# Kernel optimization log

Measured on AMD Instinct MI355X. Metric: run time of the kernel, lower is better.

## Reference

```python
import jax, jax.numpy as jnp
import numpy as np

B, N, C = 2, 2048, 1024
H = 16
D = C // H  # head_dim = 64
SCALE = D ** -0.5


def setup_inputs() -> dict:
    key = jax.random.key(0)
    ks = jax.random.split(key, 9)
    s = C ** -0.5  # ~ torch Linear default init scale
    return {
        "x": jax.random.normal(ks[0], (B, N, C), dtype=jnp.float32),
        "Wq": jax.random.uniform(ks[1], (C, C), jnp.float32, -s, s),
        "bq": jax.random.uniform(ks[2], (C,), jnp.float32, -s, s),
        "Wk": jax.random.uniform(ks[3], (C, C), jnp.float32, -s, s),
        "bk": jax.random.uniform(ks[4], (C,), jnp.float32, -s, s),
        "Wv": jax.random.uniform(ks[5], (C, C), jnp.float32, -s, s),
        "bv": jax.random.uniform(ks[6], (C,), jnp.float32, -s, s),
        "Wo": jax.random.uniform(ks[7], (C, C), jnp.float32, -s, s),
        "bo": jax.random.uniform(ks[8], (C,), jnp.float32, -s, s),
    }


def reference(x, Wq, bq, Wk, bk, Wv, bv, Wo, bo):
    # Projections: [B,N,C] -> [B,H,N,D]
    def split_heads(t):
        return t.reshape(B, N, H, D).transpose(0, 2, 1, 3)

    q = split_heads(x @ Wq.T + bq)
    k = split_heads(x @ Wk.T + bk)
    v = split_heads(x @ Wv.T + bv)

    scores = jnp.einsum("bhnd,bhmd->bhnm", q, k) * SCALE  # [B,H,N,N]
    attn = jax.nn.softmax(scores, axis=-1)
    out = jnp.einsum("bhnm,bhmd->bhnd", attn, v)  # [B,H,N,D]
    out = out.transpose(0, 2, 1, 3).reshape(B, N, C)
    return out @ Wo.T + bo
```

## Files before the change

kernel.cpp:

```cpp
#include <hip/hip_runtime.h>
#include <stdint.h>


typedef _Float16 h8 __attribute__((ext_vector_type(8)));
typedef _Float16 h4 __attribute__((ext_vector_type(4)));
typedef float f4 __attribute__((ext_vector_type(4)));
typedef float f16f __attribute__((ext_vector_type(16)));
typedef uint32_t u32;
typedef u32 u32x4 __attribute__((ext_vector_type(4)));

#define AS1(p) ((const __attribute__((address_space(1))) void*)(p))
#define AS3(p) ((__attribute__((address_space(3))) void*)(p))

template <int ITERS>
__device__ __forceinline__ void stage128B(const _Float16* g, int ldk, _Float16* s, int tid) {
#pragma unroll
  for (int j = 0; j < ITERS; ++j) {
    int off = j * 4096 + tid * 16;
    int row = off >> 7;
    int ch = (off >> 4) & 7;
    int gch = ch ^ (row & 7);
    __builtin_amdgcn_global_load_lds(AS1(g + row * ldk + gch * 8), AS3(s + (off >> 1)), 16, 0, 0);
  }
}

__device__ __forceinline__ void stage_v(const _Float16* g, _Float16* s, int tid) {
#pragma unroll
  for (int j = 0; j < 2; ++j) {
    int off = j * 4096 + tid * 16;
    int row = off >> 7;
    int ch = (off >> 4) & 7;
    int gch = ch ^ (row & 7);
    __builtin_amdgcn_global_load_lds(AS1(g + row * 2048 + gch * 8), AS3(s + (off >> 1)), 16, 0, 0);
  }
}
__device__ __forceinline__ void stage_k(const _Float16* g, _Float16* s, int tid) {
#pragma unroll
  for (int j = 0; j < 2; ++j) {
    int off = j * 4096 + tid * 16;
    int row = off >> 7;
    int ch = (off >> 4) & 7;
    int gch = ch ^ ((row & 3) | ((row >> 1) & 4));
    __builtin_amdgcn_global_load_lds(AS1(g + row * 64 + gch * 8), AS3(s + (off >> 1)), 16, 0, 0);
  }
}

__device__ __forceinline__ h8 frag64(const _Float16* s, int row, int g) {
  return *(const h8*)(s + row * 64 + ((g ^ (row & 7)) << 3));
}

__global__ void cvt_all(const float* __restrict__ x, const float* __restrict__ Wq,
                        const float* __restrict__ Wk, const float* __restrict__ Wv,
                        const float* __restrict__ Wo, _Float16* __restrict__ xh,
                        _Float16* __restrict__ q, _Float16* __restrict__ k,
                        _Float16* __restrict__ v, _Float16* __restrict__ o) {
  int blk = blockIdx.x;
  const float* src; _Float16* dst; int off;
  if (blk < 4096)      { src = x;  dst = xh; off = blk; }
  else if (blk < 5120) { src = Wq; dst = q;  off = blk - 4096; }
  else if (blk < 6144) { src = Wk; dst = k;  off = blk - 5120; }
  else if (blk < 7168) { src = Wv; dst = v;  off = blk - 6144; }
  else                 { src = Wo; dst = o;  off = blk - 7168; }
  int i = off * 1024 + threadIdx.x * 4;
  f4 vv = *(const f4*)(src + i);
  h4 ov;
  ov[0] = (_Float16)vv[0]; ov[1] = (_Float16)vv[1]; ov[2] = (_Float16)vv[2]; ov[3] = (_Float16)vv[3];
  *(h4*)(dst + i) = ov;
}

__global__ __launch_bounds__(256, 3) void gemm_qkv(
    const _Float16* __restrict__ X,
    const _Float16* __restrict__ W0, const _Float16* __restrict__ W1, const _Float16* __restrict__ W2,
    const float* __restrict__ b0, const float* __restrict__ b1, const float* __restrict__ b2,
    _Float16* __restrict__ O0, _Float16* __restrict__ O1, _Float16* __restrict__ O2) {
  __shared__ _Float16 As[128 * 64];
  __shared__ _Float16 Bs[128 * 64];
  int z = blockIdx.z;
  const _Float16* W = (z == 0) ? W0 : (z == 1) ? W1 : W2;
  const float* bias = (z == 0) ? b0 : (z == 1) ? b1 : b2;

  int tid = threadIdx.x;
  int lane = tid & 63, wave = tid >> 6;
  int quad = lane >> 4, l15 = lane & 15;
  int wm = (wave >> 1) << 6, wn = (wave & 1) << 6;
  int m0 = blockIdx.y << 7, n0 = blockIdx.x << 7;

  f4 acc[4][4] = {};
  for (int k0 = 0; k0 < 1024; k0 += 64) {
    stage128B<4>(X + m0 * 1024 + k0, 1024, As, tid);
    stage128B<4>(W + n0 * 1024 + k0, 1024, Bs, tid);
    __syncthreads();
#pragma unroll
    for (int ks = 0; ks < 2; ++ks) {
      h8 af[4], bf[4];
#pragma unroll
      for (int i = 0; i < 4; ++i) af[i] = frag64(As, wm + i * 16 + l15, ks * 4 + quad);
#pragma unroll
      for (int i = 0; i < 4; ++i) bf[i] = frag64(Bs, wn + i * 16 + l15, ks * 4 + quad);
#pragma unroll
      for (int mi = 0; mi < 4; ++mi)
#pragma unroll
        for (int ni = 0; ni < 4; ++ni)
          acc[mi][ni] = __builtin_amdgcn_mfma_f32_16x16x32_f16(af[mi], bf[ni], acc[mi][ni], 0, 0, 0);
    }
    __syncthreads();
  }

  if (z == 2) {
#pragma unroll
    for (int mi = 0; mi < 4; ++mi) {
#pragma unroll
      for (int ni = 0; ni < 4; ++ni) {
        int o = n0 + wn + ni * 16 + l15;
        float bv = bias[o];
        int h = o >> 6, dd = o & 63;
        int m = m0 + wm + mi * 16 + quad * 4;
        int b = m >> 11, n = m & 2047;
        h4 v;
#pragma unroll
        for (int r = 0; r < 4; ++r) v[r] = (_Float16)(acc[mi][ni][r] + bv);
        *(h4*)(O2 + (((b * 16 + h) * 64 + dd) * 2048 + n)) = v;
      }
    }
  } else {
    float scale = (z == 0) ? 0.125f * 1.44269504089f : 1.0f;
    _Float16* Out = (z == 0) ? O0 : O1;
#pragma unroll
    for (int mi = 0; mi < 4; ++mi) {
#pragma unroll
      for (int ni = 0; ni < 4; ++ni) {
        int o = n0 + wn + ni * 16 + l15;
        float bv = bias[o];
        int h = o >> 6, d = o & 63;
#pragma unroll
        for (int r = 0; r < 4; ++r) {
          int m = m0 + wm + mi * 16 + quad * 4 + r;
          int b = m >> 11, n = m & 2047;
          float v = (acc[mi][ni][r] + bv) * scale;
          Out[(((b * 16 + h) * 2048 + n) << 6) + d] = (_Float16)v;
        }
      }
    }
  }
}

__global__ __launch_bounds__(256, 3) void gemm_out(
    const _Float16* __restrict__ A, const _Float16* __restrict__ W,
    const float* __restrict__ bias, float* __restrict__ Out) {
  __shared__ _Float16 As[128 * 64];
  __shared__ _Float16 Bs[64 * 64];
  int tid = threadIdx.x;
  int lane = tid & 63, wave = tid >> 6;
  int quad = lane >> 4, l15 = lane & 15;
  int wm = (wave >> 1) << 6, wn = (wave & 1) << 5;
  int m0 = blockIdx.y << 7, n0 = blockIdx.x << 6;

  f4 acc[4][2] = {};
  for (int k0 = 0; k0 < 1024; k0 += 64) {
    stage128B<4>(A + m0 * 1024 + k0, 1024, As, tid);
    stage128B<2>(W + n0 * 1024 + k0, 1024, Bs, tid);
    __syncthreads();
#pragma unroll
    for (int ks = 0; ks < 2; ++ks) {
      h8 af[4], bf[2];
#pragma unroll
      for (int i = 0; i < 4; ++i) af[i] = frag64(As, wm + i * 16 + l15, ks * 4 + quad);
#pragma unroll
      for (int i = 0; i < 2; ++i) bf[i] = frag64(Bs, wn + i * 16 + l15, ks * 4 + quad);
#pragma unroll
      for (int mi = 0; mi < 4; ++mi)
#pragma unroll
        for (int ni = 0; ni < 2; ++ni)
          acc[mi][ni] = __builtin_amdgcn_mfma_f32_16x16x32_f16(af[mi], bf[ni], acc[mi][ni], 0, 0, 0);
    }
    __syncthreads();
  }
#pragma unroll
  for (int mi = 0; mi < 4; ++mi) {
#pragma unroll
    for (int ni = 0; ni < 2; ++ni) {
      int o = n0 + wn + ni * 16 + l15;
      float bv = bias[o];
#pragma unroll
      for (int r = 0; r < 4; ++r) {
        int m = m0 + wm + mi * 16 + quad * 4 + r;
        Out[m * 1024 + o] = acc[mi][ni][r] + bv;
      }
    }
  }
}

__global__ __launch_bounds__(256, 2) void attn(
    const _Float16* __restrict__ Q, const _Float16* __restrict__ Kv,
    const _Float16* __restrict__ Vt, _Float16* __restrict__ AO) {
  __shared__ _Float16 smem[8 * 4096];
  _Float16* Ksb = smem;
  _Float16* Vsb = smem + 4 * 4096;

  int tid = threadIdx.x, lane = tid & 63, wave = tid >> 6;
  int h = lane >> 5, l31 = lane & 31;
  int p = wave & 1, qg = wave >> 1;

  int flat = blockIdx.y * 16 + blockIdx.x;
  int nid = (flat & 7) * 64 + (flat >> 3);
  int bh = nid >> 4, q0 = (nid & 15) << 7;

  const _Float16* Qb = Q + (bh * 2048 + q0 + qg * 64 + l31) * 64;
  h8 qf[2][4];
#pragma unroll
  for (int qs = 0; qs < 2; ++qs)
#pragma unroll
    for (int ks4 = 0; ks4 < 4; ++ks4)
      qf[qs][ks4] = *(const h8*)(Qb + qs * 32 * 64 + ks4 * 16 + h * 8);

  int krow = (l31 & 19) | ((l31 & 4) << 1) | ((l31 & 8) >> 1);
  int kbase = (p * 32 + krow) * 64;
  int kx = (krow & 3) | ((krow >> 1) & 4);
  int vx = l31 & 7;

  const _Float16* Kb = Kv + bh * 131072;
  const _Float16* Vb = Vt + bh * 131072;

  f16f zero = {};
  f16f oacc[2][2] = {};
  float lsum0 = 0.f, lsum1 = 0.f;

  auto SMPV = [&](const f16f& sa, const f16f& sb, const _Float16* Vst) {
    u32 pkw0[8], pkw1[8];
#pragma unroll
    for (int i = 0; i < 8; ++i) {
      float pa = __builtin_amdgcn_exp2f(sa[2 * i]);
      float pb = __builtin_amdgcn_exp2f(sa[2 * i + 1]);
      lsum0 += pa + pb;
      pkw0[i] = __builtin_bit_cast(u32, __builtin_amdgcn_cvt_pkrtz(pa, pb));
      float pc = __builtin_amdgcn_exp2f(sb[2 * i]);
      float pd = __builtin_amdgcn_exp2f(sb[2 * i + 1]);
      lsum1 += pc + pd;
      pkw1[i] = __builtin_bit_cast(u32, __builtin_amdgcn_cvt_pkrtz(pc, pd));
    }
#pragma unroll
    for (int s = 0; s < 2; ++s) {
      u32x4 pw0 = {pkw0[4 * s], pkw0[4 * s + 1], pkw0[4 * s + 2], pkw0[4 * s + 3]};
      u32x4 pw1 = {pkw1[4 * s], pkw1[4 * s + 1], pkw1[4 * s + 2], pkw1[4 * s + 3]};
      h8 pb0 = __builtin_bit_cast(h8, pw0);
      h8 pb1 = __builtin_bit_cast(h8, pw1);
      int ch = (((p << 2) | (s << 1) | h) ^ vx) << 3;
      __builtin_amdgcn_s_setprio(1);
#pragma unroll
      for (int dt = 0; dt < 2; ++dt) {
        h8 vf = *(const h8*)(Vst + (dt * 32 + l31) * 64 + ch);
        oacc[0][dt] = __builtin_amdgcn_mfma_f32_32x32x16_f16(vf, pb0, oacc[0][dt], 0, 0, 0);
        oacc[1][dt] = __builtin_amdgcn_mfma_f32_32x32x16_f16(vf, pb1, oacc[1][dt], 0, 0, 0);
      }
      __builtin_amdgcn_s_setprio(0);
    }
  };

  auto QK = [&](const _Float16* Kst, f16f& s0, f16f& s1) {
    s0 = zero; s1 = zero;
    __builtin_amdgcn_s_setprio(1);
#pragma unroll
    for (int ks4 = 0; ks4 < 4; ++ks4) {
      h8 kf = *(const h8*)(Kst + kbase + (((ks4 * 2 + h) ^ kx) << 3));
      s0 = __builtin_amdgcn_mfma_f32_32x32x16_f16(kf, qf[0][ks4], s0, 0, 0, 0);
      s1 = __builtin_amdgcn_mfma_f32_32x32x16_f16(kf, qf[1][ks4], s1, 0, 0, 0);
    }
    __builtin_amdgcn_s_setprio(0);
  };

  stage_k(Kb, Ksb, tid);
  stage_v(Vb, Vsb, tid);
  stage_k(Kb + 4096, Ksb + 4096, tid);
  stage_v(Vb + 64, Vsb + 4096, tid);

  f16f sA0 = zero, sA1 = zero, sB0 = zero, sB1 = zero;

  for (int it = 0; it < 16; ++it) {
    int base = (it & 1) << 1;
    int ob = base ^ 2;
    int ph0 = it << 1;

    asm volatile("s_waitcnt vmcnt(4)\n\ts_barrier" ::: "memory");
    if (it < 15) {
      stage_k(Kb + (ph0 + 2) * 4096, Ksb + ob * 4096, tid);
      stage_v(Vb + (ph0 + 2) * 64, Vsb + ob * 4096, tid);
    }
    QK(Ksb + base * 4096, sA0, sA1);
    if (it > 0) SMPV(sB0, sB1, Vsb + (ob | 1) * 4096);

    if (it < 15) {
      asm volatile("s_waitcnt vmcnt(4)\n\ts_barrier" ::: "memory");
      stage_k(Kb + (ph0 + 3) * 4096, Ksb + (ob | 1) * 4096, tid);
      stage_v(Vb + (ph0 + 3) * 64, Vsb + (ob | 1) * 4096, tid);
    } else {
      asm volatile("s_waitcnt vmcnt(0)\n\ts_barrier" ::: "memory");
    }
    QK(Ksb + (base | 1) * 4096, sB0, sB1);
    SMPV(sA0, sA1, Vsb + base * 4096);
  }
  SMPV(sB0, sB1, Vsb + 3 * 4096);

  __syncthreads();
  float* cb = (float*)smem;
  if (p) {
    float* w = cb + (qg * 64 + lane) * 66;
#pragma unroll
    for (int qs = 0; qs < 2; ++qs)
#pragma unroll
      for (int dt = 0; dt < 2; ++dt)
#pragma unroll
        for (int i = 0; i < 16; ++i) w[(qs * 2 + dt) * 16 + i] = oacc[qs][dt][i];
    w[64] = lsum0;
    w[65] = lsum1;
  }
  __syncthreads();
  if (!p) {
    const float* r = cb + (qg * 64 + lane) * 66;
#pragma unroll
    for (int qs = 0; qs < 2; ++qs)
#pragma unroll
      for (int dt = 0; dt < 2; ++dt)
#pragma unroll
        for (int i = 0; i < 16; ++i) oacc[qs][dt][i] += r[(qs * 2 + dt) * 16 + i];
    lsum0 += r[64];
    lsum1 += r[65];

    int b = bh >> 4, hh = bh & 15;
#pragma unroll
    for (int qs = 0; qs < 2; ++qs) {
      float ls = qs ? lsum1 : lsum0;
      float l = ls + __shfl_xor(ls, 32);
      float inv = 1.0f / l;
      int n = q0 + qg * 64 + qs * 32 + l31;
      _Float16* base_ = AO + (b * 2048 + n) * 1024 + hh * 64;
#pragma unroll
      for (int dt = 0; dt < 2; ++dt) {
#pragma unroll
        for (int b2 = 0; b2 < 4; ++b2) {
          h4 o;
#pragma unroll
          for (int a = 0; a < 4; ++a) o[a] = (_Float16)(oacc[qs][dt][b2 * 4 + a] * inv);
          *(h4*)(base_ + dt * 32 + b2 * 8 + h * 4) = o;
        }
      }
    }
  }
}

extern "C" void kernel_launch(void* const* d_in, const int* in_sizes, int n_in,
                              void* d_out, int out_size, void* d_ws, size_t ws_size,
                              hipStream_t stream) {
  const float* x = (const float*)d_in[0];
  const float* Wq = (const float*)d_in[1];
  const float* bq = (const float*)d_in[2];
  const float* Wk = (const float*)d_in[3];
  const float* bk = (const float*)d_in[4];
  const float* Wv = (const float*)d_in[5];
  const float* bv = (const float*)d_in[6];
  const float* Wo = (const float*)d_in[7];
  const float* bo = (const float*)d_in[8];
  float* out = (float*)d_out;

  char* w = (char*)d_ws;
  _Float16* xh  = (_Float16*)(w);
  _Float16* Wqh = (_Float16*)(w + (8u << 20));
  _Float16* Wkh = (_Float16*)(w + (10u << 20));
  _Float16* Wvh = (_Float16*)(w + (12u << 20));
  _Float16* Woh = (_Float16*)(w + (14u << 20));
  _Float16* Qh  = (_Float16*)(w + (16u << 20));
  _Float16* Kh  = (_Float16*)(w + (24u << 20));
  _Float16* Vth = (_Float16*)(w + (32u << 20));
  _Float16* AOh = xh;

  cvt_all<<<8192, 256, 0, stream>>>(x, Wq, Wk, Wv, Wo, xh, Wqh, Wkh, Wvh, Woh);
  gemm_qkv<<<dim3(8, 32, 3), 256, 0, stream>>>(xh, Wqh, Wkh, Wvh, bq, bk, bv, Qh, Kh, Vth);
  attn<<<dim3(16, 32), 256, 0, stream>>>(Qh, Kh, Vth, AOh);
  gemm_out<<<dim3(16, 32), 256, 0, stream>>>(AOh, Woh, bo, out);
}
```

Before: 173.6 us.

## Stagger QK and PV phases across wave groups instead of setprio software pipelining

Replaces the unrolled two-phase software pipeline, which relied on s_setprio around the MFMA blocks, with a single 32-phase loop over a 4-slot ring buffer. Waves with p==0 do QK then PV on the same tile, while waves with p==1 do PV on the previous tile and then QK on the current one. Running opposite phases on different waves is meant to let exp/softmax VALU work on one wave overlap MFMA work on another. It also removes the priority hints, drops the zero-init of score accumulators, and adds a p-dependent branch that may affect register use and scheduling.

```diff
diff --git a/kernel.cpp b/kernel.cpp
--- a/kernel.cpp
+++ b/kernel.cpp
@@ -221,7 +221,6 @@
   const _Float16* Kb = Kv + bh * 131072;
   const _Float16* Vb = Vt + bh * 131072;
 
-  f16f zero = {};
   f16f oacc[2][2] = {};
   float lsum0 = 0.f, lsum1 = 0.f;
 
@@ -245,27 +244,24 @@
       h8 pb0 = __builtin_bit_cast(h8, pw0);
       h8 pb1 = __builtin_bit_cast(h8, pw1);
       int ch = (((p << 2) | (s << 1) | h) ^ vx) << 3;
-      __builtin_amdgcn_s_setprio(1);
 #pragma unroll
       for (int dt = 0; dt < 2; ++dt) {
         h8 vf = *(const h8*)(Vst + (dt * 32 + l31) * 64 + ch);
         oacc[0][dt] = __builtin_amdgcn_mfma_f32_32x32x16_f16(vf, pb0, oacc[0][dt], 0, 0, 0);
         oacc[1][dt] = __builtin_amdgcn_mfma_f32_32x32x16_f16(vf, pb1, oacc[1][dt], 0, 0, 0);
       }
-      __builtin_amdgcn_s_setprio(0);
     }
   };
 
   auto QK = [&](const _Float16* Kst, f16f& s0, f16f& s1) {
-    s0 = zero; s1 = zero;
-    __builtin_amdgcn_s_setprio(1);
+    f16f a = {}, b = {};
 #pragma unroll
     for (int ks4 = 0; ks4 < 4; ++ks4) {
       h8 kf = *(const h8*)(Kst + kbase + (((ks4 * 2 + h) ^ kx) << 3));
-      s0 = __builtin_amdgcn_mfma_f32_32x32x16_f16(kf, qf[0][ks4], s0, 0, 0, 0);
-      s1 = __builtin_amdgcn_mfma_f32_32x32x16_f16(kf, qf[1][ks4], s1, 0, 0, 0);
-    }
-    __builtin_amdgcn_s_setprio(0);
+      a = __builtin_amdgcn_mfma_f32_32x32x16_f16(kf, qf[0][ks4], a, 0, 0, 0);
+      b = __builtin_amdgcn_mfma_f32_32x32x16_f16(kf, qf[1][ks4], b, 0, 0, 0);
+    }
+    s0 = a; s1 = b;
   };
 
   stage_k(Kb, Ksb, tid);
@@ -273,32 +269,30 @@
   stage_k(Kb + 4096, Ksb + 4096, tid);
   stage_v(Vb + 64, Vsb + 4096, tid);
 
-  f16f sA0 = zero, sA1 = zero, sB0 = zero, sB1 = zero;
-
-  for (int it = 0; it < 16; ++it) {
-    int base = (it & 1) << 1;
-    int ob = base ^ 2;
-    int ph0 = it << 1;
-
-    asm volatile("s_waitcnt vmcnt(4)\n\ts_barrier" ::: "memory");
-    if (it < 15) {
-      stage_k(Kb + (ph0 + 2) * 4096, Ksb + ob * 4096, tid);
-      stage_v(Vb + (ph0 + 2) * 64, Vsb + ob * 4096, tid);
-    }
-    QK(Ksb + base * 4096, sA0, sA1);
-    if (it > 0) SMPV(sB0, sB1, Vsb + (ob | 1) * 4096);
-
-    if (it < 15) {
+  f16f sP0, sP1;
+
+  for (int ph = 0; ph < 32; ++ph) {
+    int sl = ph & 3;
+    if (ph < 31) {
       asm volatile("s_waitcnt vmcnt(4)\n\ts_barrier" ::: "memory");
-      stage_k(Kb + (ph0 + 3) * 4096, Ksb + (ob | 1) * 4096, tid);
-      stage_v(Vb + (ph0 + 3) * 64, Vsb + (ob | 1) * 4096, tid);
     } else {
       asm volatile("s_waitcnt vmcnt(0)\n\ts_barrier" ::: "memory");
     }
-    QK(Ksb + (base | 1) * 4096, sB0, sB1);
-    SMPV(sA0, sA1, Vsb + base * 4096);
-  }
-  SMPV(sB0, sB1, Vsb + 3 * 4096);
+    if (ph < 30) {
+      int so = (ph + 2) & 3;
+      stage_k(Kb + (ph + 2) * 4096, Ksb + so * 4096, tid);
+      stage_v(Vb + (ph + 2) * 64, Vsb + so * 4096, tid);
+    }
+    if (p == 0) {
+      f16f s0, s1;
+      QK(Ksb + sl * 4096, s0, s1);
+      SMPV(s0, s1, Vsb + sl * 4096);
+    } else {
+      if (ph > 0) SMPV(sP0, sP1, Vsb + ((ph - 1) & 3) * 4096);
+      QK(Ksb + sl * 4096, sP0, sP1);
+    }
+  }
+  if (p) SMPV(sP0, sP1, Vsb + 3 * 4096);
 
   __syncthreads();
   float* cb = (float*)smem;
```

Result: slower. 182.6 us (+5.1%).
